# Optimization experiments

Hardware: AMD Instinct MI355X
Metric: run time of the kernel (lower is better)

## Reference

```python
import jax, jax.numpy as jnp
import numpy as np

NEG_INF = -1e9
LRELU_SLOPE = 0.2

B, C, FIN, FOUT = 8, 2048, 128, 64


def setup_inputs() -> dict:
    key = jax.random.key(0)
    k1, k2, k3, k4 = jax.random.split(key, 4)
    H = jax.random.normal(k1, (B, C, FIN), dtype=jnp.float32)
    A = jax.random.randint(k2, (B, C, C), 0, 2, dtype=jnp.int32)
    W = jax.random.normal(k3, (FIN, FOUT), dtype=jnp.float32)
    a = jax.random.normal(k4, (2 * FOUT,), dtype=jnp.float32)
    return {"H": H, "A": A, "W": W, "a": a}


def reference(H, A, W, a):
    # Wh: [B, C, F]
    Wh = jnp.einsum("bcf,fo->bco", H, W)
    F = Wh.shape[-1]
    a1, a2 = a[:F], a[F:]
    # e_ij = a . concat(Wh_i, Wh_j) = (Wh_i . a1) + (Wh_j . a2)
    # -> never materialize the (B,C,C,2F) concat tensor; same math.
    s1 = jnp.einsum("bcf,f->bc", Wh, a1)  # [B, C] contribution of node i
    s2 = jnp.einsum("bcf,f->bc", Wh, a2)  # [B, C] contribution of node j
    e = jax.nn.leaky_relu(s1[:, :, None] + s2[:, None, :], LRELU_SLOPE)  # [B,C,C]
    mask = (A > 0) | jnp.eye(A.shape[-1], dtype=bool)[None]
    e = jnp.where(mask, e, NEG_INF)
    alpha = jax.nn.softmax(e, axis=-1)
    # dropout omitted (eval mode) for a deterministic correctness baseline
    out = jax.nn.relu(jnp.einsum("bij,bjf->bif", alpha, Wh))
    return out
```

## Files before the change

### kernel.cpp

```cpp
#include <hip/hip_runtime.h>

#define NB 8
#define NC 2048
#define KIN 128
#define NF 64

#define WTSTRIDE 136
#define RSTRIDE 68
#define MROW 272
#define MOFF 60.0f
#define LOG2E 1.44269504088896340736f

typedef float floatx4_t __attribute__((ext_vector_type(4)));
typedef __bf16 bf16x8_t __attribute__((ext_vector_type(8)));
typedef unsigned short ushort8_t __attribute__((ext_vector_type(8)));

static __device__ __forceinline__ unsigned short f2bf(float f) {
  union { float f; unsigned int u; } v; v.f = f;
  unsigned int u = v.u;
  u += 0x7FFFu + ((u >> 16) & 1u);
  return (unsigned short)(u >> 16);
}

static __device__ __forceinline__ float lrelu(float x) {
  return fmaxf(x, 0.2f * x);
}

__global__ __launch_bounds__(256, 4) void k0_mask(
    const int* __restrict__ A, unsigned char* __restrict__ maskG)
{
  const int wv = blockIdx.x * 4 + (threadIdx.x >> 6);
  const int lane = threadIdx.x & 63;
  const int r = wv & (NC - 1);
  const int* arow = A + (size_t)wv * NC;

  int4 v[8];
#pragma unroll
  for (int s = 0; s < 4; ++s) {
    const int cbase = s * 512 + lane * 8;
    v[2 * s]     = *(const int4*)(arow + cbase);
    v[2 * s + 1] = *(const int4*)(arow + cbase + 4);
  }

  unsigned char* mrow = maskG + (size_t)wv * 256;
#pragma unroll
  for (int s = 0; s < 4; ++s) {
    const int cbase = s * 512 + lane * 8;
    const int4 a0 = v[2 * s];
    const int4 a1 = v[2 * s + 1];
    unsigned int byte = 0;
    byte |= (a0.x > 0 || cbase + 0 == r) ? 1u : 0u;
    byte |= (a0.y > 0 || cbase + 1 == r) ? 2u : 0u;
    byte |= (a0.z > 0 || cbase + 2 == r) ? 4u : 0u;
    byte |= (a0.w > 0 || cbase + 3 == r) ? 8u : 0u;
    byte |= (a1.x > 0 || cbase + 4 == r) ? 16u : 0u;
    byte |= (a1.y > 0 || cbase + 5 == r) ? 32u : 0u;
    byte |= (a1.z > 0 || cbase + 6 == r) ? 64u : 0u;
    byte |= (a1.w > 0 || cbase + 7 == r) ? 128u : 0u;
    mrow[s * 64 + lane] = (unsigned char)byte;
  }
}

__global__ __launch_bounds__(256, 4) void k1_prep(
    const float* __restrict__ H, const float* __restrict__ W,
    const float* __restrict__ avec,
    float* __restrict__ s1g, float* __restrict__ s2g,
    unsigned short* __restrict__ WhT)
{
  __shared__ unsigned short WTsh[NF * WTSTRIDE];
  __shared__ float w1sh[KIN];
  __shared__ float w2sh[KIN];

  const int t = threadIdx.x;
  const int b = blockIdx.x >> 7;
  const int c0 = (blockIdx.x & 127) * 16;

  for (int i = t; i < KIN * NF; i += 256) {
    int k = i >> 6, f = i & 63;
    WTsh[f * WTSTRIDE + k] = f2bf(W[i]);
  }
  if (t < KIN) {
    float acc1 = 0.f, acc2 = 0.f;
    const float* wr = W + t * NF;
#pragma unroll
    for (int f = 0; f < NF; ++f) {
      float wv = wr[f];
      acc1 += wv * avec[f];
      acc2 += wv * avec[NF + f];
    }
    w1sh[t] = acc1;
    w2sh[t] = acc2;
  }
  __syncthreads();

  {
    const int r = t >> 4;
    const int x = t & 15;
    const float* hp = H + (size_t)(b * NC + c0 + r) * KIN + x * 8;
    float4 h0 = *(const float4*)(hp);
    float4 h1 = *(const float4*)(hp + 4);
    float4 u10 = *(const float4*)(w1sh + x * 8);
    float4 u11 = *(const float4*)(w1sh + x * 8 + 4);
    float4 u20 = *(const float4*)(w2sh + x * 8);
    float4 u21 = *(const float4*)(w2sh + x * 8 + 4);
    float p1 = h0.x * u10.x + h0.y * u10.y + h0.z * u10.z + h0.w * u10.w
             + h1.x * u11.x + h1.y * u11.y + h1.z * u11.z + h1.w * u11.w;
    float p2 = h0.x * u20.x + h0.y * u20.y + h0.z * u20.z + h0.w * u20.w
             + h1.x * u21.x + h1.y * u21.y + h1.z * u21.z + h1.w * u21.w;
#pragma unroll
    for (int off = 1; off < 16; off <<= 1) {
      p1 += __shfl_xor(p1, off);
      p2 += __shfl_xor(p2, off);
    }
    if (x == 0) {
      s1g[b * NC + c0 + r] = p1;
      s2g[b * NC + c0 + r] = p2;
    }
  }

  const int wave = t >> 6;
  const int lane = t & 63;
  const int m = lane & 15;
  const int q = lane >> 4;
  floatx4_t acc = (floatx4_t){0.f, 0.f, 0.f, 0.f};

  const float* hb = H + (size_t)(b * NC + c0 + m) * KIN;
#pragma unroll
  for (int kt = 0; kt < 4; ++kt) {
    const int kbase = kt * 32 + q * 8;
    float4 h0 = *(const float4*)(hb + kbase);
    float4 h1 = *(const float4*)(hb + kbase + 4);
    ushort8_t bu;
    bu[0] = f2bf(h0.x); bu[1] = f2bf(h0.y); bu[2] = f2bf(h0.z); bu[3] = f2bf(h0.w);
    bu[4] = f2bf(h1.x); bu[5] = f2bf(h1.y); bu[6] = f2bf(h1.z); bu[7] = f2bf(h1.w);
    bf16x8_t bf = __builtin_bit_cast(bf16x8_t, bu);
    ushort8_t au = *(const ushort8_t*)(WTsh + (wave * 16 + m) * WTSTRIDE + kbase);
    bf16x8_t af = __builtin_bit_cast(bf16x8_t, au);
    acc = __builtin_amdgcn_mfma_f32_16x16x32_bf16(af, bf, acc, 0, 0, 0);
  }
#pragma unroll
  for (int i2 = 0; i2 < 4; ++i2) {
    const int f = wave * 16 + q * 4 + i2;
    WhT[(size_t)(b * NF + f) * NC + c0 + m] = f2bf(acc[i2]);
  }
}

__global__ __launch_bounds__(256, 4) void k2_attn(
    const unsigned char* __restrict__ maskG, const float* __restrict__ s1g,
    const float* __restrict__ s2g, const unsigned short* __restrict__ WhT,
    float* __restrict__ out)
{
  __shared__ float s2_sh[NC];
  __shared__ unsigned char mask_sh[16 * MROW];
  __shared__ float s1_sh[16];
  __shared__ float wmax_sh[4];
  __shared__ float red_sh[4 * 16 * RSTRIDE];
  __shared__ float lsum_sh[4 * 16];

  const int t = threadIdx.x;
  const int b = blockIdx.x >> 7;
  const int i0 = (blockIdx.x & 127) * 16;
  const int wave = t >> 6;
  const int lane = t & 63;

  float lmax;
  {
    const float* sp = s2g + b * NC;
    float4 v0 = *(const float4*)(sp + t * 4);
    float4 v1 = *(const float4*)(sp + 1024 + t * 4);
    *(float4*)(s2_sh + t * 4) = v0;
    *(float4*)(s2_sh + 1024 + t * 4) = v1;
    lmax = fmaxf(fmaxf(fmaxf(v0.x, v0.y), fmaxf(v0.z, v0.w)),
                 fmaxf(fmaxf(v1.x, v1.y), fmaxf(v1.z, v1.w)));
#pragma unroll
    for (int off = 1; off < 64; off <<= 1)
      lmax = fmaxf(lmax, __shfl_xor(lmax, off));
    if (lane == 0) wmax_sh[wave] = lmax;
  }
  if (t < 16) s1_sh[t] = s1g[b * NC + i0 + t];

  {
    const int row = t >> 4;
    const int off = (t & 15) * 16;
    const uint4 mv =
        *(const uint4*)(maskG + (size_t)(b * NC + i0 + row) * 256 + off);
    *(uint4*)(mask_sh + row * MROW + off) = mv;
  }
  __syncthreads();

  const float s2max =
      fmaxf(fmaxf(wmax_sh[0], wmax_sh[1]), fmaxf(wmax_sh[2], wmax_sh[3]));

  const int m = lane & 15;
  const int q = lane >> 4;
  const float s1m = s1_sh[m];
  const float mmL = (lrelu(s1m + s2max) - MOFF) * LOG2E;
  const unsigned short* whb = WhT + (size_t)b * NF * NC;

  ushort8_t ou;
  {
    const unsigned short ov = (m == 0) ? (unsigned short)0x3F80 : (unsigned short)0;
#pragma unroll
    for (int idx = 0; idx < 8; ++idx) ou[idx] = ov;
  }
  const bf16x8_t onesf = __builtin_bit_cast(bf16x8_t, ou);

  floatx4_t acc[4], accl;
#pragma unroll
  for (int nt = 0; nt < 4; ++nt) acc[nt] = (floatx4_t){0.f, 0.f, 0.f, 0.f};
  accl = (floatx4_t){0.f, 0.f, 0.f, 0.f};

  const int ktBeg = wave * 16;
  for (int kk = 0; kk < 16; ++kk) {
    const int kt = ktBeg + kk;
    const int jq = kt * 32 + q * 8;
    const unsigned int mb = mask_sh[m * MROW + kt * 4 + q];
    ushort8_t whc[4];
#pragma unroll
    for (int nt = 0; nt < 4; ++nt)
      whc[nt] = *(const ushort8_t*)(whb + (size_t)(nt * 16 + m) * NC + jq);

    float4 s0 = *(const float4*)(s2_sh + jq);
    float4 s1v = *(const float4*)(s2_sh + jq + 4);
    const float sv[8] = {s0.x, s0.y, s0.z, s0.w, s1v.x, s1v.y, s1v.z, s1v.w};
    uint4 pk;
#pragma unroll
    for (int pair = 0; pair < 4; ++pair) {
      float p0 = __builtin_amdgcn_exp2f(
          fmaf(lrelu(s1m + sv[2 * pair]), LOG2E, -mmL));
      float p1 = __builtin_amdgcn_exp2f(
          fmaf(lrelu(s1m + sv[2 * pair + 1]), LOG2E, -mmL));
      p0 = (mb & (1u << (2 * pair))) ? p0 : 0.0f;
      p1 = (mb & (2u << (2 * pair))) ? p1 : 0.0f;
      pk[pair] = __builtin_amdgcn_perm(__builtin_bit_cast(unsigned int, p1),
                                       __builtin_bit_cast(unsigned int, p0),
                                       0x07060302u);
    }
    const bf16x8_t af = __builtin_bit_cast(bf16x8_t, pk);
#pragma unroll
    for (int nt = 0; nt < 4; ++nt) {
      bf16x8_t bf = __builtin_bit_cast(bf16x8_t, whc[nt]);
      acc[nt] = __builtin_amdgcn_mfma_f32_16x16x32_bf16(af, bf, acc[nt], 0, 0, 0);
    }
    accl = __builtin_amdgcn_mfma_f32_16x16x32_bf16(af, onesf, accl, 0, 0, 0);
  }

#pragma unroll
  for (int nt = 0; nt < 4; ++nt) {
#pragma unroll
    for (int i2 = 0; i2 < 4; ++i2) {
      red_sh[wave * (16 * RSTRIDE) + (q * 4 + i2) * RSTRIDE + nt * 16 + m] =
          acc[nt][i2];
    }
  }
  if (m == 0) {
#pragma unroll
    for (int i2 = 0; i2 < 4; ++i2)
      lsum_sh[wave * 16 + q * 4 + i2] = accl[i2];
  }
  __syncthreads();

  {
    const int row = t >> 4;
    const int f0 = (t & 15) * 4;
    float4 v = {0.f, 0.f, 0.f, 0.f};
    float ls = 0.f;
#pragma unroll
    for (int w = 0; w < 4; ++w) {
      const float* rp = red_sh + w * (16 * RSTRIDE) + row * RSTRIDE + f0;
      float4 vv = *(const float4*)rp;
      v.x += vv.x; v.y += vv.y; v.z += vv.z; v.w += vv.w;
      ls += lsum_sh[w * 16 + row];
    }
    const float inv = 1.0f / ls;
    float4 o;
    o.x = fmaxf(v.x * inv, 0.f);
    o.y = fmaxf(v.y * inv, 0.f);
    o.z = fmaxf(v.z * inv, 0.f);
    o.w = fmaxf(v.w * inv, 0.f);
    *(float4*)(out + (size_t)(b * NC + i0 + row) * NF + f0) = o;
  }
}

extern "C" void kernel_launch(void* const* d_in, const int* in_sizes, int n_in,
                              void* d_out, int out_size, void* d_ws, size_t ws_size,
                              hipStream_t stream) {
  const float* H = (const float*)d_in[0];
  const int* A = (const int*)d_in[1];
  const float* W = (const float*)d_in[2];
  const float* avec = (const float*)d_in[3];
  float* out = (float*)d_out;

  char* ws = (char*)d_ws;
  unsigned short* WhT = (unsigned short*)ws;
  float* s1 = (float*)(ws + (size_t)NB * NF * NC * 2);
  float* s2 = s1 + NB * NC;
  unsigned char* maskG = (unsigned char*)(s2 + NB * NC);

  k0_mask<<<dim3(NB * NC / 4), dim3(256), 0, stream>>>(A, maskG);
  k1_prep<<<dim3(NB * (NC / 16)), dim3(256), 0, stream>>>(H, W, avec, s1, s2, WhT);
  k2_attn<<<dim3(NB * (NC / 16)), dim3(256), 0, stream>>>(maskG, s1, s2, WhT, out);
}
```

Before: 241.5 us.

## Split attention work by feature slice per wave with fragment-ordered Wh layout

k1 now writes Wh in an MFMA-fragment-ordered layout, so each lane of k2 can stream its B operand with one contiguous 16-byte load. Loads are prefetched through a four-deep register ring. k2 now handles 32 rows per block, and each wave owns 16 output features across the full key range instead of a quarter of the keys across all features. That removes the cross-wave shared-memory reduction and a barrier, and lowers launch bounds to two blocks per CU. The cost is that every wave recomputes the exp/mask probability tile for all 2048 keys, which multiplies the VALU exp work per row by four.

```diff
diff --git a/kernel.cpp b/kernel.cpp
--- a/kernel.cpp
+++ b/kernel.cpp
@@ -6,7 +6,6 @@
 #define NF 64
 
 #define WTSTRIDE 136
-#define RSTRIDE 68
 #define MROW 272
 #define MOFF 60.0f
 #define LOG2E 1.44269504088896340736f
@@ -65,7 +64,7 @@
     const float* __restrict__ H, const float* __restrict__ W,
     const float* __restrict__ avec,
     float* __restrict__ s1g, float* __restrict__ s2g,
-    unsigned short* __restrict__ WhT)
+    unsigned short* __restrict__ WhT3)
 {
   __shared__ unsigned short WTsh[NF * WTSTRIDE];
   __shared__ float w1sh[KIN];
@@ -138,28 +137,31 @@
     bf16x8_t af = __builtin_bit_cast(bf16x8_t, au);
     acc = __builtin_amdgcn_mfma_f32_16x16x32_bf16(af, bf, acc, 0, 0, 0);
   }
-#pragma unroll
-  for (int i2 = 0; i2 < 4; ++i2) {
-    const int f = wave * 16 + q * 4 + i2;
-    WhT[(size_t)(b * NF + f) * NC + c0 + m] = f2bf(acc[i2]);
-  }
-}
-
-__global__ __launch_bounds__(256, 4) void k2_attn(
+  {
+    const int c = c0 + m;
+    const int ktc = c >> 5, q2 = (c >> 3) & 3, j = c & 7;
+    unsigned short* base =
+        WhT3 + ((((size_t)(b * 4 + wave) * 64 + ktc) * 4 + q2) * 16) * 8 + j;
+#pragma unroll
+    for (int i2 = 0; i2 < 4; ++i2)
+      base[(q * 4 + i2) * 8] = f2bf(acc[i2]);
+  }
+}
+
+__global__ __launch_bounds__(256, 2) void k2_attn(
     const unsigned char* __restrict__ maskG, const float* __restrict__ s1g,
-    const float* __restrict__ s2g, const unsigned short* __restrict__ WhT,
+    const float* __restrict__ s2g, const unsigned short* __restrict__ WhT3,
     float* __restrict__ out)
 {
   __shared__ float s2_sh[NC];
-  __shared__ unsigned char mask_sh[16 * MROW];
-  __shared__ float s1_sh[16];
+  __shared__ unsigned char mask_sh[32 * MROW];
+  __shared__ float s1_sh[32];
   __shared__ float wmax_sh[4];
-  __shared__ float red_sh[4 * 16 * RSTRIDE];
-  __shared__ float lsum_sh[4 * 16];
+  __shared__ float lsum_sh[4 * 32];
 
   const int t = threadIdx.x;
-  const int b = blockIdx.x >> 7;
-  const int i0 = (blockIdx.x & 127) * 16;
+  const int b = blockIdx.x >> 6;
+  const int i0 = (blockIdx.x & 63) * 32;
   const int wave = t >> 6;
   const int lane = t & 63;
 
@@ -177,14 +179,14 @@
       lmax = fmaxf(lmax, __shfl_xor(lmax, off));
     if (lane == 0) wmax_sh[wave] = lmax;
   }
-  if (t < 16) s1_sh[t] = s1g[b * NC + i0 + t];
-
-  {
-    const int row = t >> 4;
-    const int off = (t & 15) * 16;
-    const uint4 mv =
-        *(const uint4*)(maskG + (size_t)(b * NC + i0 + row) * 256 + off);
-    *(uint4*)(mask_sh + row * MROW + off) = mv;
+  if (t < 32) s1_sh[t] = s1g[b * NC + i0 + t];
+
+  {
+    const int row = t >> 3;
+    const int off = (t & 7) * 32;
+    const unsigned char* src = maskG + (size_t)(b * NC + i0 + row) * 256 + off;
+    *(uint4*)(mask_sh + row * MROW + off) = *(const uint4*)(src);
+    *(uint4*)(mask_sh + row * MROW + off + 16) = *(const uint4*)(src + 16);
   }
   __syncthreads();
 
@@ -193,9 +195,10 @@
 
   const int m = lane & 15;
   const int q = lane >> 4;
-  const float s1m = s1_sh[m];
-  const float mmL = (lrelu(s1m + s2max) - MOFF) * LOG2E;
-  const unsigned short* whb = WhT + (size_t)b * NF * NC;
+  const float s1A = s1_sh[m];
+  const float s1B = s1_sh[16 + m];
+  const float mmLA = (lrelu(s1A + s2max) - MOFF) * LOG2E;
+  const float mmLB = (lrelu(s1B + s2max) - MOFF) * LOG2E;
 
   ushort8_t ou;
   {
@@ -205,80 +208,76 @@
   }
   const bf16x8_t onesf = __builtin_bit_cast(bf16x8_t, ou);
 
-  floatx4_t acc[4], accl;
-#pragma unroll
-  for (int nt = 0; nt < 4; ++nt) acc[nt] = (floatx4_t){0.f, 0.f, 0.f, 0.f};
-  accl = (floatx4_t){0.f, 0.f, 0.f, 0.f};
-
-  const int ktBeg = wave * 16;
-  for (int kk = 0; kk < 16; ++kk) {
-    const int kt = ktBeg + kk;
+  floatx4_t accA = {0.f, 0.f, 0.f, 0.f}, accB = {0.f, 0.f, 0.f, 0.f};
+  floatx4_t acclA = {0.f, 0.f, 0.f, 0.f}, acclB = {0.f, 0.f, 0.f, 0.f};
+
+  const unsigned short* wstream =
+      WhT3 + ((size_t)(b * 4 + wave) * 64) * 512 + (size_t)lane * 8;
+  ushort8_t wbuf[4];
+#pragma unroll
+  for (int i = 0; i < 4; ++i)
+    wbuf[i] = *(const ushort8_t*)(wstream + i * 512);
+
+#pragma unroll 4
+  for (int kt = 0; kt < 64; ++kt) {
+    const ushort8_t wcur = wbuf[kt & 3];
+    if (kt + 4 < 64)
+      wbuf[kt & 3] = *(const ushort8_t*)(wstream + (kt + 4) * 512);
+
     const int jq = kt * 32 + q * 8;
-    const unsigned int mb = mask_sh[m * MROW + kt * 4 + q];
-    ushort8_t whc[4];
-#pragma unroll
-    for (int nt = 0; nt < 4; ++nt)
-      whc[nt] = *(const ushort8_t*)(whb + (size_t)(nt * 16 + m) * NC + jq);
-
+    const unsigned int mbA = mask_sh[m * MROW + kt * 4 + q];
+    const unsigned int mbB = mask_sh[(m + 16) * MROW + kt * 4 + q];
     float4 s0 = *(const float4*)(s2_sh + jq);
     float4 s1v = *(const float4*)(s2_sh + jq + 4);
     const float sv[8] = {s0.x, s0.y, s0.z, s0.w, s1v.x, s1v.y, s1v.z, s1v.w};
-    uint4 pk;
+
+    uint4 pkA, pkB;
 #pragma unroll
     for (int pair = 0; pair < 4; ++pair) {
-      float p0 = __builtin_amdgcn_exp2f(
-          fmaf(lrelu(s1m + sv[2 * pair]), LOG2E, -mmL));
-      float p1 = __builtin_amdgcn_exp2f(
-          fmaf(lrelu(s1m + sv[2 * pair + 1]), LOG2E, -mmL));
-      p0 = (mb & (1u << (2 * pair))) ? p0 : 0.0f;
-      p1 = (mb & (2u << (2 * pair))) ? p1 : 0.0f;
-      pk[pair] = __builtin_amdgcn_perm(__builtin_bit_cast(unsigned int, p1),
-                                       __builtin_bit_cast(unsigned int, p0),
-                                       0x07060302u);
-    }
-    const bf16x8_t af = __builtin_bit_cast(bf16x8_t, pk);
-#pragma unroll
-    for (int nt = 0; nt < 4; ++nt) {
-      bf16x8_t bf = __builtin_bit_cast(bf16x8_t, whc[nt]);
-      acc[nt] = __builtin_amdgcn_mfma_f32_16x16x32_bf16(af, bf, acc[nt], 0, 0, 0);
-    }
-    accl = __builtin_amdgcn_mfma_f32_16x16x32_bf16(af, onesf, accl, 0, 0, 0);
-  }
-
-#pragma unroll
-  for (int nt = 0; nt < 4; ++nt) {
+      float a0 = __builtin_amdgcn_exp2f(
+          fmaf(lrelu(s1A + sv[2 * pair]), LOG2E, -mmLA));
+      float a1 = __builtin_amdgcn_exp2f(
+          fmaf(lrelu(s1A + sv[2 * pair + 1]), LOG2E, -mmLA));
+      float b0 = __builtin_amdgcn_exp2f(
+          fmaf(lrelu(s1B + sv[2 * pair]), LOG2E, -mmLB));
+      float b1 = __builtin_amdgcn_exp2f(
+          fmaf(lrelu(s1B + sv[2 * pair + 1]), LOG2E, -mmLB));
+      a0 = (mbA & (1u << (2 * pair))) ? a0 : 0.0f;
+      a1 = (mbA & (2u << (2 * pair))) ? a1 : 0.0f;
+      b0 = (mbB & (1u << (2 * pair))) ? b0 : 0.0f;
+      b1 = (mbB & (2u << (2 * pair))) ? b1 : 0.0f;
+      pkA[pair] = __builtin_amdgcn_perm(__builtin_bit_cast(unsigned int, a1),
+                                        __builtin_bit_cast(unsigned int, a0),
+                                        0x07060302u);
+      pkB[pair] = __builtin_amdgcn_perm(__builtin_bit_cast(unsigned int, b1),
+                                        __builtin_bit_cast(unsigned int, b0),
+                                        0x07060302u);
+    }
+    const bf16x8_t afA = __builtin_bit_cast(bf16x8_t, pkA);
+    const bf16x8_t afB = __builtin_bit_cast(bf16x8_t, pkB);
+    const bf16x8_t bfc = __builtin_bit_cast(bf16x8_t, wcur);
+    accA = __builtin_amdgcn_mfma_f32_16x16x32_bf16(afA, bfc, accA, 0, 0, 0);
+    acclA = __builtin_amdgcn_mfma_f32_16x16x32_bf16(afA, onesf, acclA, 0, 0, 0);
+    accB = __builtin_amdgcn_mfma_f32_16x16x32_bf16(afB, bfc, accB, 0, 0, 0);
+    acclB = __builtin_amdgcn_mfma_f32_16x16x32_bf16(afB, onesf, acclB, 0, 0, 0);
+  }
+
+  if (m == 0) {
 #pragma unroll
     for (int i2 = 0; i2 < 4; ++i2) {
-      red_sh[wave * (16 * RSTRIDE) + (q * 4 + i2) * RSTRIDE + nt * 16 + m] =
-          acc[nt][i2];
-    }
-  }
-  if (m == 0) {
-#pragma unroll
-    for (int i2 = 0; i2 < 4; ++i2)
-      lsum_sh[wave * 16 + q * 4 + i2] = accl[i2];
-  }
-  __syncthreads();
-
-  {
-    const int row = t >> 4;
-    const int f0 = (t & 15) * 4;
-    float4 v = {0.f, 0.f, 0.f, 0.f};
-    float ls = 0.f;
-#pragma unroll
-    for (int w = 0; w < 4; ++w) {
-      const float* rp = red_sh + w * (16 * RSTRIDE) + row * RSTRIDE + f0;
-      float4 vv = *(const float4*)rp;
-      v.x += vv.x; v.y += vv.y; v.z += vv.z; v.w += vv.w;
-      ls += lsum_sh[w * 16 + row];
-    }
-    const float inv = 1.0f / ls;
-    float4 o;
-    o.x = fmaxf(v.x * inv, 0.f);
-    o.y = fmaxf(v.y * inv, 0.f);
-    o.z = fmaxf(v.z * inv, 0.f);
-    o.w = fmaxf(v.w * inv, 0.f);
-    *(float4*)(out + (size_t)(b * NC + i0 + row) * NF + f0) = o;
+      lsum_sh[wave * 32 + q * 4 + i2] = acclA[i2];
+      lsum_sh[wave * 32 + 16 + q * 4 + i2] = acclB[i2];
+    }
+  }
+
+#pragma unroll
+  for (int i2 = 0; i2 < 4; ++i2) {
+    const float invA = 1.0f / lsum_sh[wave * 32 + q * 4 + i2];
+    const float invB = 1.0f / lsum_sh[wave * 32 + 16 + q * 4 + i2];
+    out[(size_t)(b * NC + i0 + q * 4 + i2) * NF + wave * 16 + m] =
+        fmaxf(accA[i2] * invA, 0.f);
+    out[(size_t)(b * NC + i0 + 16 + q * 4 + i2) * NF + wave * 16 + m] =
+        fmaxf(accB[i2] * invB, 0.f);
   }
 }
 
@@ -292,12 +291,12 @@
   float* out = (float*)d_out;
 
   char* ws = (char*)d_ws;
-  unsigned short* WhT = (unsigned short*)ws;
+  unsigned short* WhT3 = (unsigned short*)ws;
   float* s1 = (float*)(ws + (size_t)NB * NF * NC * 2);
   float* s2 = s1 + NB * NC;
   unsigned char* maskG = (unsigned char*)(s2 + NB * NC);
 
   k0_mask<<<dim3(NB * NC / 4), dim3(256), 0, stream>>>(A, maskG);
-  k1_prep<<<dim3(NB * (NC / 16)), dim3(256), 0, stream>>>(H, W, avec, s1, s2, WhT);
-  k2_attn<<<dim3(NB * (NC / 16)), dim3(256), 0, stream>>>(maskG, s1, s2, WhT, out);
-}
+  k1_prep<<<dim3(NB * (NC / 16)), dim3(256), 0, stream>>>(H, W, avec, s1, s2, WhT3);
+  k2_attn<<<dim3(NB * (NC / 32)), dim3(256), 0, stream>>>(maskG, s1, s2, WhT3, out);
+}
```

Result: slower. 248.6 us (+2.9%).
